# Optimization experiments

Measured on AMD Instinct MI355X. Metric: run time of the kernel, lower is better.

The kernel has to match this reference:

```python
import jax, jax.numpy as jnp
import numpy as np

B, T, D = 16, 4096, 256


def setup_inputs() -> dict:
    key = jax.random.key(0)
    ks = jax.random.split(key, 10)
    s = 1.0 / np.sqrt(D)  # torch nn.Linear default init range
    inp = {
        "x": jax.random.normal(ks[0], (B, T, D), jnp.float32),
        "hidden": jax.random.normal(ks[1], (B, D), jnp.float32),
    }
    names = ["W0", "b0", "W1", "b1", "W2", "b2", "W3", "b3"]
    for i, n in enumerate(names):
        shape = (D, D) if n.startswith("W") else (D,)
        inp[n] = jax.random.uniform(ks[2 + i], shape, jnp.float32, -s, s)
    return inp


def _gln(x, W0, b0, W1, b1, W2, b2, W3, b3):
    # Two gated-linear blocks; the final Linear(hyper[-1], hidden_size) in the
    # original module is never applied by calc_gln (index == len-1 is skipped).
    h = (x @ W0.T + b0) * jax.nn.sigmoid(x @ W1.T + b1)
    return (h @ W2.T + b2) * jax.nn.sigmoid(h @ W3.T + b3)


def reference(x, hidden, W0, b0, W1, b1, W2, b2, W3, b3):
    b = _gln(x, W0, b0, W1, b1, W2, b2, W3, b3)  # [B, T, D]
    bt = jnp.swapaxes(b, 0, 1)  # [T, B, D] for time-major scan
    init = jax.nn.relu(bt[0] + jnp.roll(hidden, 1, -1))

    def step(prev, b_t):
        out = jax.nn.relu(b_t + jnp.roll(prev, 1, -1))
        return out, out

    last, ys = jax.lax.scan(step, init, bt[1:])
    outputs = jnp.concatenate([init[None], ys], axis=0)  # [T, B, D]
    outputs = jnp.swapaxes(outputs, 0, 1)  # [B, T, D]; squeeze(2) is a no-op for D>1
    return outputs, last
```

## Files before the change

kernel.cpp:

```cpp
#include <hip/hip_runtime.h>
#include <hip/hip_bf16.h>
#include <cstdint>
#include <cstddef>

typedef __bf16 bf16x8 __attribute__((ext_vector_type(8)));
typedef float  f32x4  __attribute__((ext_vector_type(4)));

static constexpr int B  = 16;
static constexpr int T  = 4096;
static constexpr int D  = 256;
static constexpr int M  = B * T;
static constexpr int SEGS = 64;
static constexpr int SEGL = T / SEGS;

__device__ __forceinline__ float sigmoid_fast(float v) {
    return __builtin_amdgcn_rcpf(1.0f + __expf(-v));
}

__global__ void cvt_w(const float* __restrict__ W0, const float* __restrict__ W1,
                      const float* __restrict__ W2, const float* __restrict__ W3,
                      __bf16* __restrict__ wp) {
    int i = blockIdx.x * blockDim.x + threadIdx.x;
    int s    = i >> 14;
    int r    = i & 16383;
    int ks   = r >> 11;
    int fg   = (r >> 6) & 31;
    int lane = r & 63;
    int kg = lane >> 4, rl = lane & 15;
    int w = fg >> 2, f = fg & 3;
    int q = f >> 1, gate = f & 1;
    int rc = w * 32 + 2 * rl + q;
    const float* src = (s == 0) ? (gate ? W1 : W0) : (gate ? W3 : W2);
    const float* p = src + (size_t)rc * 256 + ks * 32 + kg * 8;
    bf16x8 o;
#pragma unroll
    for (int j = 0; j < 8; ++j) o[j] = (__bf16)p[j];
    *reinterpret_cast<bf16x8*>(wp + (size_t)s * 131072 +
                               ((size_t)((ks * 32 + fg) * 64 + lane)) * 8) = o;
}

__launch_bounds__(512, 4)
__global__ void gln_fused(const float* __restrict__ x,
                          const __bf16* __restrict__ wp,
                          const float* __restrict__ b0, const float* __restrict__ b1,
                          const float* __restrict__ b2, const float* __restrict__ b3,
                          float* __restrict__ out,
                          float2* __restrict__ seg_am) {
    __shared__ char tile[32768];

    const int tid  = threadIdx.x;
    const int lane = tid & 63;
    const int wid  = tid >> 6;
    const int rl   = lane & 15;
    const int kg   = lane >> 4;
    const int row0 = blockIdx.x * 64;

    const __bf16* wv0 = wp + ((size_t)(wid * 4) * 64 + lane) * 8;
    const __bf16* wv1 = wv0 + 131072;

    bf16x8 bbuf[2][4];
    auto loadB = [&](int p, const __bf16* wvb, int ks) {
#pragma unroll
        for (int f = 0; f < 4; ++f)
            bbuf[p][f] = *reinterpret_cast<const bf16x8*>(wvb + ks * 16384 + f * 512);
    };

    {
        int r  = tid >> 3;
        int c0 = tid & 7;
        const float* xr = x + (size_t)(row0 + r) * 256;
        float4 xa[4][2];
#pragma unroll
        for (int ci = 0; ci < 4; ++ci) {
            const float4* p = reinterpret_cast<const float4*>(xr + (c0 + ci * 8) * 8);
            xa[ci][0] = p[0];
            xa[ci][1] = p[1];
        }
#pragma unroll
        for (int ci = 0; ci < 4; ++ci) {
            int ck = c0 + ci * 8;
            int pc = ck ^ ((r & 7) << 2);
            bf16x8 o = { (__bf16)xa[ci][0].x, (__bf16)xa[ci][0].y,
                         (__bf16)xa[ci][0].z, (__bf16)xa[ci][0].w,
                         (__bf16)xa[ci][1].x, (__bf16)xa[ci][1].y,
                         (__bf16)xa[ci][1].z, (__bf16)xa[ci][1].w };
            *reinterpret_cast<bf16x8*>(&tile[r * 512 + pc * 16]) = o;
        }
    }
    loadB(0, wv0, 0);
    __syncthreads();

    f32x4 acc[4][4];

    auto run_stage = [&](const __bf16* wvb) {
#pragma unroll
        for (int m = 0; m < 4; ++m)
#pragma unroll
            for (int f = 0; f < 4; ++f) acc[m][f] = (f32x4){0.f, 0.f, 0.f, 0.f};
#pragma unroll
        for (int ks = 0; ks < 8; ++ks) {
            if (ks < 7) loadB((ks + 1) & 1, wvb, ks + 1);
            bf16x8 aR[4];
#pragma unroll
            for (int m = 0; m < 4; ++m) {
                int row = m * 16 + rl;
                int pc  = (ks * 4 + kg) ^ ((row & 7) << 2);
                aR[m] = *reinterpret_cast<const bf16x8*>(&tile[row * 512 + pc * 16]);
            }
#pragma unroll
            for (int m = 0; m < 4; ++m)
#pragma unroll
                for (int f = 0; f < 4; ++f)
                    acc[m][f] = __builtin_amdgcn_mfma_f32_16x16x32_bf16(
                        aR[m], bbuf[ks & 1][f], acc[m][f], 0, 0, 0);
        }
    };

    const int rc0 = wid * 32 + 2 * rl;

    run_stage(wv0);
    loadB(0, wv1, 0);
    __syncthreads();
    {
        float2 bb0 = *reinterpret_cast<const float2*>(b0 + rc0);
        float2 bb1 = *reinterpret_cast<const float2*>(b1 + rc0);
        int cb  = rc0 * 2;
        int ck  = cb >> 4;
        int off = cb & 15;
#pragma unroll
        for (int m = 0; m < 4; ++m)
#pragma unroll
            for (int j = 0; j < 4; ++j) {
                int row = m * 16 + kg * 4 + j;
                float he = (acc[m][0][j] + bb0.x) * sigmoid_fast(acc[m][1][j] + bb1.x);
                float ho = (acc[m][2][j] + bb0.y) * sigmoid_fast(acc[m][3][j] + bb1.y);
                unsigned short ue = __builtin_bit_cast(unsigned short, (__bf16)he);
                unsigned short uo = __builtin_bit_cast(unsigned short, (__bf16)ho);
                unsigned int u = ((unsigned int)uo << 16) | (unsigned int)ue;
                int pc = ck ^ ((row & 7) << 2);
                *reinterpret_cast<unsigned int*>(&tile[row * 512 + pc * 16 + off]) = u;
            }
    }
    __syncthreads();

    run_stage(wv1);

    float2 ov[16];
    {
        float2 bb2 = *reinterpret_cast<const float2*>(b2 + rc0);
        float2 bb3 = *reinterpret_cast<const float2*>(b3 + rc0);
#pragma unroll
        for (int m = 0; m < 4; ++m)
#pragma unroll
            for (int j = 0; j < 4; ++j) {
                float he = (acc[m][0][j] + bb2.x) * sigmoid_fast(acc[m][1][j] + bb3.x);
                float ho = (acc[m][2][j] + bb2.y) * sigmoid_fast(acc[m][3][j] + bb3.y);
                float2 o; o.x = he; o.y = ho;
                ov[m * 4 + j] = o;
            }
    }
    __syncthreads();

    float* ftile = reinterpret_cast<float*>(tile);
#pragma unroll
    for (int m = 0; m < 2; ++m)
#pragma unroll
        for (int j = 0; j < 4; ++j) {
            int row = m * 16 + kg * 4 + j;
            int col = rc0 ^ ((row & 7) << 2);
            *reinterpret_cast<float2*>(&ftile[row * 256 + col]) = ov[m * 4 + j];
        }
    __syncthreads();

    const int batch = row0 >> 12;
    const int t0    = row0 & 4095;
    const int seg   = t0 >> 6;
    float A = 0.f, Mx = -1e30f;
    int cc = 0;
    if (tid < 256) {
        cc = (tid + t0) & 255;
#pragma unroll 8
        for (int i = 0; i < 32; ++i) {
            int col = ((cc + i) & 255) ^ ((i & 7) << 2);
            float v = ftile[i * 256 + col];
            A += v;
            Mx = fmaxf(Mx + v, 0.f);
        }
    }
    __syncthreads();
#pragma unroll
    for (int m = 2; m < 4; ++m)
#pragma unroll
        for (int j = 0; j < 4; ++j) {
            int row = m * 16 + kg * 4 + j;
            int pr  = row & 31;
            int col = rc0 ^ ((pr & 7) << 2);
            *reinterpret_cast<float2*>(&ftile[pr * 256 + col]) = ov[m * 4 + j];
        }
    __syncthreads();

#pragma unroll
    for (int m = 0; m < 4; ++m)
#pragma unroll
        for (int j = 0; j < 4; ++j) {
            int row = m * 16 + kg * 4 + j;
            *reinterpret_cast<float2*>(out + (size_t)(row0 + row) * 256 + rc0) =
                ov[m * 4 + j];
        }

    if (tid < 256) {
#pragma unroll 8
        for (int i = 32; i < 64; ++i) {
            int pr  = i - 32;
            int col = ((cc + i) & 255) ^ ((pr & 7) << 2);
            float v = ftile[pr * 256 + col];
            A += v;
            Mx = fmaxf(Mx + v, 0.f);
        }
        float2 o; o.x = A; o.y = Mx;
        seg_am[(size_t)(batch * SEGS + seg) * 256 + tid] = o;
    }
}

__global__ void scan_apply(float* __restrict__ bio,
                           const float2* __restrict__ seg_am,
                           const float* __restrict__ hidden,
                           float* __restrict__ last) {
    int tid   = blockIdx.x * blockDim.x + threadIdx.x;
    int c     = tid & 255;
    int rest  = tid >> 8;
    int batch = rest & 15;
    int seg   = rest >> 4;
    float s = hidden[batch * 256 + ((c + 255) & 255)];
    const float2* am = seg_am + ((size_t)batch * SEGS) * 256 + c;
    for (int k = 0; k < seg; ++k) {
        float2 a = am[(size_t)k * 256];
        s = fmaxf(s + a.x, a.y);
    }
    float* base = bio + (size_t)batch * T * D;
    int t0 = seg * SEGL;
#pragma unroll 8
    for (int i = 0; i < SEGL; ++i) {
        int t = t0 + i;
        size_t idx = (size_t)t * 256 + ((c + t) & 255);
        float v = base[idx];
        s = fmaxf(s + v, 0.f);
        base[idx] = s;
    }
    if (seg == SEGS - 1) last[batch * 256 + ((c + 255) & 255)] = s;
}

extern "C" void kernel_launch(void* const* d_in, const int* in_sizes, int n_in,
                              void* d_out, int out_size, void* d_ws, size_t ws_size,
                              hipStream_t stream) {
    const float* x      = (const float*)d_in[0];
    const float* hidden = (const float*)d_in[1];
    const float* W0 = (const float*)d_in[2];
    const float* b0 = (const float*)d_in[3];
    const float* W1 = (const float*)d_in[4];
    const float* b1 = (const float*)d_in[5];
    const float* W2 = (const float*)d_in[6];
    const float* b2 = (const float*)d_in[7];
    const float* W3 = (const float*)d_in[8];
    const float* b3 = (const float*)d_in[9];

    float* out  = (float*)d_out;
    float* last = out + (size_t)M * D;

    char* ws = (char*)d_ws;
    __bf16* wpb    = (__bf16*)ws;
    float2* seg_am = (float2*)(ws + 524288);

    cvt_w<<<128, 256, 0, stream>>>(W0, W1, W2, W3, wpb);
    gln_fused<<<M / 64, 512, 0, stream>>>(x, wpb, b0, b1, b2, b3, out, seg_am);
    scan_apply<<<(B * D * SEGS) / 256, 256, 0, stream>>>(out, seg_am, hidden, last);
}
```

Before: 84.30 us.

## Process two row tiles per block and prefetch the second tile's x

Each block now handles two 64-row tiles with double-buffered LDS, launching half as many blocks. The global load of the second tile's x is issued during the first tile's epilogue, so its latency overlaps compute. __syncthreads is replaced by raw s_barrier plus explicit lgkmcnt waits to cut barrier overhead. The cost is 64KB of LDS per block, which limits occupancy, plus fewer blocks for load balance and a risk of missing vmem waits around the raw barriers.

```diff
diff --git a/kernel.cpp b/kernel.cpp
--- a/kernel.cpp
+++ b/kernel.cpp
@@ -12,6 +12,11 @@
 static constexpr int M  = B * T;
 static constexpr int SEGS = 64;
 static constexpr int SEGL = T / SEGS;
+
+#define RBAR() do { asm volatile("" ::: "memory"); \
+                    __builtin_amdgcn_s_barrier();  \
+                    asm volatile("" ::: "memory"); } while (0)
+#define LGKM0() asm volatile("s_waitcnt lgkmcnt(0)" ::: "memory")
 
 __device__ __forceinline__ float sigmoid_fast(float v) {
     return __builtin_amdgcn_rcpf(1.0f + __expf(-v));
@@ -46,18 +51,23 @@
                           const float* __restrict__ b2, const float* __restrict__ b3,
                           float* __restrict__ out,
                           float2* __restrict__ seg_am) {
-    __shared__ char tile[32768];
+    __shared__ char tiles[2][32768];
 
     const int tid  = threadIdx.x;
     const int lane = tid & 63;
     const int wid  = tid >> 6;
     const int rl   = lane & 15;
     const int kg   = lane >> 4;
-    const int row0 = blockIdx.x * 64;
+    const int row0A = blockIdx.x * 128;
+    const int row0B = row0A + 64;
 
     const __bf16* wv0 = wp + ((size_t)(wid * 4) * 64 + lane) * 8;
     const __bf16* wv1 = wv0 + 131072;
 
+    const int r   = tid >> 3;
+    const int c0  = tid & 7;
+    const int rc0 = wid * 32 + 2 * rl;
+
     bf16x8 bbuf[2][4];
     auto loadB = [&](int p, const __bf16* wvb, int ks) {
 #pragma unroll
@@ -65,34 +75,31 @@
             bbuf[p][f] = *reinterpret_cast<const bf16x8*>(wvb + ks * 16384 + f * 512);
     };
 
-    {
-        int r  = tid >> 3;
-        int c0 = tid & 7;
-        const float* xr = x + (size_t)(row0 + r) * 256;
-        float4 xa[4][2];
+    float4 xr[4][2];
+    auto issue_x = [&](int row0t) {
+        const float* xp = x + (size_t)(row0t + r) * 256;
 #pragma unroll
         for (int ci = 0; ci < 4; ++ci) {
-            const float4* p = reinterpret_cast<const float4*>(xr + (c0 + ci * 8) * 8);
-            xa[ci][0] = p[0];
-            xa[ci][1] = p[1];
-        }
+            const float4* p = reinterpret_cast<const float4*>(xp + (c0 + ci * 8) * 8);
+            xr[ci][0] = p[0];
+            xr[ci][1] = p[1];
+        }
+    };
+    auto write_x = [&](char* tbuf) {
 #pragma unroll
         for (int ci = 0; ci < 4; ++ci) {
             int ck = c0 + ci * 8;
             int pc = ck ^ ((r & 7) << 2);
-            bf16x8 o = { (__bf16)xa[ci][0].x, (__bf16)xa[ci][0].y,
-                         (__bf16)xa[ci][0].z, (__bf16)xa[ci][0].w,
-                         (__bf16)xa[ci][1].x, (__bf16)xa[ci][1].y,
-                         (__bf16)xa[ci][1].z, (__bf16)xa[ci][1].w };
-            *reinterpret_cast<bf16x8*>(&tile[r * 512 + pc * 16]) = o;
-        }
-    }
-    loadB(0, wv0, 0);
-    __syncthreads();
+            bf16x8 o = { (__bf16)xr[ci][0].x, (__bf16)xr[ci][0].y,
+                         (__bf16)xr[ci][0].z, (__bf16)xr[ci][0].w,
+                         (__bf16)xr[ci][1].x, (__bf16)xr[ci][1].y,
+                         (__bf16)xr[ci][1].z, (__bf16)xr[ci][1].w };
+            *reinterpret_cast<bf16x8*>(&tbuf[r * 512 + pc * 16]) = o;
+        }
+    };
 
     f32x4 acc[4][4];
-
-    auto run_stage = [&](const __bf16* wvb) {
+    auto run_stage = [&](const char* alds, const __bf16* wvb) {
 #pragma unroll
         for (int m = 0; m < 4; ++m)
 #pragma unroll
@@ -105,7 +112,7 @@
             for (int m = 0; m < 4; ++m) {
                 int row = m * 16 + rl;
                 int pc  = (ks * 4 + kg) ^ ((row & 7) << 2);
-                aR[m] = *reinterpret_cast<const bf16x8*>(&tile[row * 512 + pc * 16]);
+                aR[m] = *reinterpret_cast<const bf16x8*>(&alds[row * 512 + pc * 16]);
             }
 #pragma unroll
             for (int m = 0; m < 4; ++m)
@@ -116,12 +123,7 @@
         }
     };
 
-    const int rc0 = wid * 32 + 2 * rl;
-
-    run_stage(wv0);
-    loadB(0, wv1, 0);
-    __syncthreads();
-    {
+    auto epi0 = [&](char* tbuf) {
         float2 bb0 = *reinterpret_cast<const float2*>(b0 + rc0);
         float2 bb1 = *reinterpret_cast<const float2*>(b1 + rc0);
         int cb  = rc0 * 2;
@@ -138,15 +140,12 @@
                 unsigned short uo = __builtin_bit_cast(unsigned short, (__bf16)ho);
                 unsigned int u = ((unsigned int)uo << 16) | (unsigned int)ue;
                 int pc = ck ^ ((row & 7) << 2);
-                *reinterpret_cast<unsigned int*>(&tile[row * 512 + pc * 16 + off]) = u;
-            }
-    }
-    __syncthreads();
-
-    run_stage(wv1);
+                *reinterpret_cast<unsigned int*>(&tbuf[row * 512 + pc * 16 + off]) = u;
+            }
+    };
 
     float2 ov[16];
-    {
+    auto epi1 = [&]() {
         float2 bb2 = *reinterpret_cast<const float2*>(b2 + rc0);
         float2 bb3 = *reinterpret_cast<const float2*>(b3 + rc0);
 #pragma unroll
@@ -158,68 +157,96 @@
                 float2 o; o.x = he; o.y = ho;
                 ov[m * 4 + j] = o;
             }
-    }
-    __syncthreads();
-
-    float* ftile = reinterpret_cast<float*>(tile);
-#pragma unroll
-    for (int m = 0; m < 2; ++m)
-#pragma unroll
-        for (int j = 0; j < 4; ++j) {
-            int row = m * 16 + kg * 4 + j;
-            int col = rc0 ^ ((row & 7) << 2);
-            *reinterpret_cast<float2*>(&ftile[row * 256 + col]) = ov[m * 4 + j];
-        }
-    __syncthreads();
-
-    const int batch = row0 >> 12;
-    const int t0    = row0 & 4095;
-    const int seg   = t0 >> 6;
-    float A = 0.f, Mx = -1e30f;
-    int cc = 0;
-    if (tid < 256) {
-        cc = (tid + t0) & 255;
+    };
+
+    auto tail = [&](char* tbuf, int row0t) {
+        float* ftile = reinterpret_cast<float*>(tbuf);
+#pragma unroll
+        for (int m = 0; m < 2; ++m)
+#pragma unroll
+            for (int j = 0; j < 4; ++j) {
+                int row = m * 16 + kg * 4 + j;
+                int col = rc0 ^ ((row & 7) << 2);
+                *reinterpret_cast<float2*>(&ftile[row * 256 + col]) = ov[m * 4 + j];
+            }
+        LGKM0(); RBAR();
+        const int batch = row0t >> 12;
+        const int t0    = row0t & 4095;
+        const int seg   = t0 >> 6;
+        float A = 0.f, Mx = -1e30f;
+        int cc = 0;
+        if (tid < 256) {
+            cc = (tid + t0) & 255;
 #pragma unroll 8
-        for (int i = 0; i < 32; ++i) {
-            int col = ((cc + i) & 255) ^ ((i & 7) << 2);
-            float v = ftile[i * 256 + col];
-            A += v;
-            Mx = fmaxf(Mx + v, 0.f);
-        }
-    }
-    __syncthreads();
-#pragma unroll
-    for (int m = 2; m < 4; ++m)
-#pragma unroll
-        for (int j = 0; j < 4; ++j) {
-            int row = m * 16 + kg * 4 + j;
-            int pr  = row & 31;
-            int col = rc0 ^ ((pr & 7) << 2);
-            *reinterpret_cast<float2*>(&ftile[pr * 256 + col]) = ov[m * 4 + j];
-        }
-    __syncthreads();
-
-#pragma unroll
-    for (int m = 0; m < 4; ++m)
-#pragma unroll
-        for (int j = 0; j < 4; ++j) {
-            int row = m * 16 + kg * 4 + j;
-            *reinterpret_cast<float2*>(out + (size_t)(row0 + row) * 256 + rc0) =
-                ov[m * 4 + j];
-        }
-
-    if (tid < 256) {
+            for (int i = 0; i < 32; ++i) {
+                int col = ((cc + i) & 255) ^ ((i & 7) << 2);
+                float v = ftile[i * 256 + col];
+                A += v;
+                Mx = fmaxf(Mx + v, 0.f);
+            }
+        }
+        RBAR();
+#pragma unroll
+        for (int m = 2; m < 4; ++m)
+#pragma unroll
+            for (int j = 0; j < 4; ++j) {
+                int row = m * 16 + kg * 4 + j;
+                int pr  = row & 31;
+                int col = rc0 ^ ((pr & 7) << 2);
+                *reinterpret_cast<float2*>(&ftile[pr * 256 + col]) = ov[m * 4 + j];
+            }
+#pragma unroll
+        for (int m = 0; m < 4; ++m)
+#pragma unroll
+            for (int j = 0; j < 4; ++j) {
+                int row = m * 16 + kg * 4 + j;
+                *reinterpret_cast<float2*>(out + (size_t)(row0t + row) * 256 + rc0) =
+                    ov[m * 4 + j];
+            }
+        LGKM0(); RBAR();
+        if (tid < 256) {
 #pragma unroll 8
-        for (int i = 32; i < 64; ++i) {
-            int pr  = i - 32;
-            int col = ((cc + i) & 255) ^ ((pr & 7) << 2);
-            float v = ftile[pr * 256 + col];
-            A += v;
-            Mx = fmaxf(Mx + v, 0.f);
-        }
-        float2 o; o.x = A; o.y = Mx;
-        seg_am[(size_t)(batch * SEGS + seg) * 256 + tid] = o;
-    }
+            for (int i = 32; i < 64; ++i) {
+                int pr  = i - 32;
+                int col = ((cc + i) & 255) ^ ((pr & 7) << 2);
+                float v = ftile[pr * 256 + col];
+                A += v;
+                Mx = fmaxf(Mx + v, 0.f);
+            }
+            float2 o; o.x = A; o.y = Mx;
+            seg_am[(size_t)(batch * SEGS + seg) * 256 + tid] = o;
+        }
+    };
+
+    issue_x(row0A);
+    write_x(tiles[0]);
+    loadB(0, wv0, 0);
+    LGKM0(); RBAR();
+
+    run_stage(tiles[0], wv0);
+    loadB(0, wv1, 0);
+    RBAR();
+    epi0(tiles[0]);
+    LGKM0(); RBAR();
+    run_stage(tiles[0], wv1);
+    epi1();
+    issue_x(row0B);
+    RBAR();
+    tail(tiles[0], row0A);
+
+    write_x(tiles[1]);
+    loadB(0, wv0, 0);
+    LGKM0(); RBAR();
+
+    run_stage(tiles[1], wv0);
+    loadB(0, wv1, 0);
+    RBAR();
+    epi0(tiles[1]);
+    LGKM0(); RBAR();
+    run_stage(tiles[1], wv1);
+    epi1();
+    RBAR();
+    tail(tiles[1], row0B);
 }
 
 __global__ void scan_apply(float* __restrict__ bio,
@@ -272,6 +299,6 @@
     float2* seg_am = (float2*)(ws + 524288);
 
     cvt_w<<<128, 256, 0, stream>>>(W0, W1, W2, W3, wpb);
-    gln_fused<<<M / 64, 512, 0, stream>>>(x, wpb, b0, b1, b2, b3, out, seg_am);
+    gln_fused<<<M / 128, 512, 0, stream>>>(x, wpb, b0, b1, b2, b3, out, seg_am);
     scan_apply<<<(B * D * SEGS) / 256, 256, 0, stream>>>(out, seg_am, hidden, last);
 }
```

Result: slower. 155.8 us (+84.8%).
